# Kernel tuning notes

Hardware: AMD Instinct MI355X
Metric: run time of the kernel (lower is better)

## Reference

```python
import jax, jax.numpy as jnp
import numpy as np

# Config mirroring NEQUIPLayerFlax(hidden_irreps='64x0e + 64x1o', max_ell=1,
# avg_num_neighbors=16.0, num_species=5, mlp_n_hidden=64, mlp_n_layers=3, active_fn='relu')
N = 20000        # nodes
E = 320000       # edges (avg degree 16)
M = 64           # multiplicity per irrep
NR = 8           # radial embedding size
NSPEC = 5
AVG_NEI = 16.0
SQRT3 = 1.7320508075688772


def setup_inputs() -> dict:
    key = jax.random.key(0)
    ks = jax.random.split(key, 16)
    f32 = jnp.float32
    return {
        "vectors": jax.random.normal(ks[0], (E, 3), f32),
        "node_feats": jax.random.normal(ks[1], (N, 4 * M), f32),  # 64x0e (64) + 64x1o (192)
        "node_specie": jax.random.randint(ks[2], (N,), 0, NSPEC, jnp.int32),
        "radial_embedding": jax.random.uniform(ks[3], (E, NR), f32),
        "senders": jax.random.randint(ks[4], (E,), 0, N, jnp.int32),
        "receivers": jax.random.randint(ks[5], (E,), 0, N, jnp.int32),
        # linear_up: per-irrep-type mixing (no bias, e3nn-style /sqrt(fan_in))
        "W_up_s": jax.random.normal(ks[6], (M, M), f32),
        "W_up_v": jax.random.normal(ks[7], (M, M), f32),
        # radial MLP: NR -> 64 -> 64 -> 64 -> num_irreps(messages)=256
        "mlp_w1": jax.random.normal(ks[8], (NR, 64), f32),
        "mlp_w2": jax.random.normal(ks[9], (64, 64), f32),
        "mlp_w3": jax.random.normal(ks[10], (64, 64), f32),
        "mlp_wo": jax.random.normal(ks[11], (64, 4 * M), f32),
        # skip_tp: species-indexed linear node_feats -> (64x0e + 64x1o + 64x0e gates)
        "W_skip_s": jax.random.normal(ks[12], (NSPEC, M, 2 * M), f32),
        "W_skip_v": jax.random.normal(ks[13], (NSPEC, M, M), f32),
        # linear_down: messages (128x0e + 128x1o) -> (128x0e + 64x1o)
        "W_down_s": jax.random.normal(ks[14], (2 * M, 2 * M), f32),
        "W_down_v": jax.random.normal(ks[15], (2 * M, M), f32),
    }


def reference(vectors, node_feats, node_specie, radial_embedding, senders, receivers,
              W_up_s, W_up_v, mlp_w1, mlp_w2, mlp_w3, mlp_wo,
              W_skip_s, W_skip_v, W_down_s, W_down_v):
    n = node_feats.shape[0]
    s = node_feats[:, :M]                          # [N, 64]   0e
    v = node_feats[:, M:].reshape(n, M, 3)         # [N, 64,3] 1o

    inv_m = 1.0 / jnp.sqrt(jnp.asarray(M, node_feats.dtype))
    up_s = (s @ W_up_s) * inv_m                    # linear_up, scalar block
    up_v = jnp.einsum('nmc,mk->nkc', v, W_up_v) * inv_m

    es = up_s[senders]                             # [E, 64]
    ev = up_v[senders]                             # [E, 64, 3]

    # Y1 spherical harmonics, normalize=True, 'component' norm -> sqrt(3) * unit vector
    lengths = jnp.linalg.norm(vectors, axis=1, keepdims=True)         # [E,1]
    y = SQRT3 * vectors / lengths                                     # [E,3]

    # tensor products kept by filter_ir_out = hidden + '0e':
    # 1o x 1o -> 0e (CG = delta/sqrt(3), component norm)
    tp_s = jnp.einsum('emc,ec->em', ev, y) / SQRT3                    # [E,64]
    # 0e x 1o -> 1o (coefficient 1 under component norm)
    tp_v = es[:, :, None] * y[:, None, :]                             # [E,64,3]

    # concatenate + regroup -> 128x0e + 128x1o
    msg_s = jnp.concatenate([es, tp_s], axis=1)                       # [E,128]
    msg_v = jnp.concatenate([ev, tp_v], axis=1)                       # [E,128,3]

    # radial MLP (silu, /sqrt(fan_in) weight norm, no output activation)
    h = jax.nn.silu((radial_embedding @ mlp_w1) / jnp.sqrt(jnp.asarray(NR, jnp.float32)))
    h = jax.nn.silu((h @ mlp_w2) / 8.0)
    h = jax.nn.silu((h @ mlp_w3) / 8.0)
    mix = (h @ mlp_wo) / 8.0                                          # [E,256] = num_irreps
    mix = jnp.where(lengths == 0.0, 0.0, mix)

    msg_s = msg_s * mix[:, :2 * M]
    msg_v = msg_v * mix[:, 2 * M:, None]

    # scatter-sum to receivers, normalize by sqrt(avg_num_neighbors)
    inv_sq_nei = 1.0 / jnp.sqrt(jnp.asarray(AVG_NEI, jnp.float32))
    agg_s = jax.ops.segment_sum(msg_s, receivers, num_segments=n) * inv_sq_nei  # [N,128]
    agg_v = jax.ops.segment_sum(msg_v, receivers, num_segments=n) * inv_sq_nei  # [N,128,3]

    # linear_down -> irreps 64x0e + 64x1o + 64x0e(gates)  (scalars packed as 128)
    inv_2m = 1.0 / jnp.sqrt(jnp.asarray(2 * M, jnp.float32))
    down_s = (agg_s @ W_down_s) * inv_2m                              # [N,128]
    down_v = jnp.einsum('nmc,mk->nkc', agg_v, W_down_v) * inv_2m      # [N,64,3]

    # species-indexed skip connection from input node_feats
    Ws = W_skip_s[node_specie]                                        # [N,64,128]
    Wv = W_skip_v[node_specie]                                        # [N,64,64]
    skip_s = jnp.einsum('nm,nmk->nk', s, Ws) * inv_m                  # [N,128]
    skip_v = jnp.einsum('nmc,nmk->nkc', v, Wv) * inv_m                # [N,64,3]

    f_s = down_s + skip_s
    f_v = down_v + skip_v

    # gate: first 64 scalars are features (even_act=silu), last 64 scalars gate the 1o's
    gated_s = jax.nn.silu(f_s[:, :M])                                 # [N,64]
    gates = jax.nn.silu(f_s[:, M:])                                   # [N,64]
    gated_v = gates[:, :, None] * f_v                                 # [N,64,3]

    out = jnp.concatenate([gated_s, gated_v.reshape(n, 3 * M)], axis=1)  # [N,256]
    return jax.nn.relu(out)  # active_fn == 'relu'
```

## Files before the change

kernel.cpp:

```cpp
#include <hip/hip_runtime.h>
#include <hip/hip_fp16.h>

#define NN 20000
#define EE 320000

typedef _Float16 f16;
typedef f16  f16x8 __attribute__((ext_vector_type(8)));
typedef float f32x4 __attribute__((ext_vector_type(4)));

__device__ __forceinline__ float silu_f(float x) {
    return x / (1.0f + __expf(-x));
}

__global__ __launch_bounds__(256) void up_kernel(
    const float* __restrict__ nf, const float* __restrict__ Wus,
    const float* __restrict__ Wuv, float* __restrict__ up, int dmajor)
{
    __shared__ float sWs[64 * 64];
    __shared__ float sWv[64 * 64];
    int tid = threadIdx.x;
    for (int i = tid; i < 64 * 64; i += 256) { sWs[i] = Wus[i]; sWv[i] = Wuv[i]; }
    __syncthreads();
    int lane = tid & 63, wv = tid >> 6;
    for (int it = 0; it < 4; it++) {
        int n = blockIdx.x * 16 + wv * 4 + it;
        const float* row = nf + (size_t)n * 256;
        float s  = row[lane];
        float v0 = row[64 + lane * 3 + 0];
        float v1 = row[64 + lane * 3 + 1];
        float v2 = row[64 + lane * 3 + 2];
        float as = 0.f, a0 = 0.f, a1 = 0.f, a2 = 0.f;
        #pragma unroll 8
        for (int m = 0; m < 64; m++) {
            float sm = __shfl(s, m);
            float b0 = __shfl(v0, m), b1 = __shfl(v1, m), b2 = __shfl(v2, m);
            float w_s = sWs[m * 64 + lane];
            float w_v = sWv[m * 64 + lane];
            as += sm * w_s;
            a0 += b0 * w_v; a1 += b1 * w_v; a2 += b2 * w_v;
        }
        float* o = up + (size_t)n * 256;
        if (dmajor) {
            o[lane]       = as * 0.125f;
            o[64  + lane] = a0 * 0.125f;
            o[128 + lane] = a1 * 0.125f;
            o[192 + lane] = a2 * 0.125f;
        } else {
            o[lane] = as * 0.125f;
            o[64 + lane * 3 + 0] = a0 * 0.125f;
            o[64 + lane * 3 + 1] = a1 * 0.125f;
            o[64 + lane * 3 + 2] = a2 * 0.125f;
        }
    }
}

__global__ __launch_bounds__(256) void pack_kernel(
    const float* __restrict__ w1, const float* __restrict__ w2,
    const float* __restrict__ w3, const float* __restrict__ wo,
    f16* __restrict__ wp)
{
    int idx = blockIdx.x * 256 + threadIdx.x;
    if (idx >= 52 * 64) return;
    int frag = idx >> 6, lane = idx & 63;
    int col = lane & 15, kg = lane >> 4;
    f16x8 pv;
    if (frag < 4) {
        int t = frag;
        #pragma unroll
        for (int i = 0; i < 8; i++) {
            int k = kg * 8 + i;
            pv[i] = (k < 8) ? (f16)w1[k * 64 + t * 16 + col] : (f16)0.f;
        }
    } else if (frag < 12) {
        int f = frag - 4, t = f >> 1, h = f & 1;
        #pragma unroll
        for (int i = 0; i < 8; i++) {
            int k = h * 32 + kg * 8 + i;
            pv[i] = (f16)w2[k * 64 + t * 16 + col];
        }
    } else if (frag < 20) {
        int f = frag - 12, t = f >> 1, h = f & 1;
        #pragma unroll
        for (int i = 0; i < 8; i++) {
            int k = h * 32 + kg * 8 + i;
            pv[i] = (f16)w3[k * 64 + t * 16 + col];
        }
    } else {
        int f = frag - 20, t = f >> 1, h = f & 1;
        #pragma unroll
        for (int i = 0; i < 8; i++) {
            int k = h * 32 + kg * 8 + i;
            pv[i] = (f16)wo[k * 256 + t * 16 + col];
        }
    }
    *(f16x8*)(wp + (size_t)idx * 8) = pv;
}

__global__ __launch_bounds__(256) void pack2_kernel(
    const float* __restrict__ Wds, const float* __restrict__ Wdv,
    const float* __restrict__ Wss, const float* __restrict__ Wsv,
    f16* __restrict__ wp2)
{
    int idx = blockIdx.x * 256 + threadIdx.x;
    if (idx >= 168 * 64) return;
    int frag = idx >> 6, lane = idx & 63;
    int col = lane & 15, kg = lane >> 4;
    const float S_d = 0.25f * 0.08838834764831845f;
    const float S_k = 0.125f;
    f16x8 pv;
    if (frag < 32) {
        int t = frag >> 2, kf = frag & 3;
        #pragma unroll
        for (int i = 0; i < 8; i++) {
            int k = kf * 32 + kg * 8 + i;
            pv[i] = (f16)(Wds[k * 128 + t * 16 + col] * S_d);
        }
    } else if (frag < 48) {
        int f = frag - 32; int t = f >> 2, kf = f & 3;
        #pragma unroll
        for (int i = 0; i < 8; i++) {
            int k = kf * 32 + kg * 8 + i;
            pv[i] = (f16)(Wdv[k * 64 + t * 16 + col] * S_d);
        }
    } else if (frag < 128) {
        int f = frag - 48; int sp = f >> 4; int t = (f & 15) >> 1; int kf = f & 1;
        #pragma unroll
        for (int i = 0; i < 8; i++) {
            int k = kf * 32 + kg * 8 + i;
            pv[i] = (f16)(Wss[((size_t)sp * 64 + k) * 128 + t * 16 + col] * S_k);
        }
    } else {
        int f = frag - 128; int sp = f >> 3; int t = (f & 7) >> 1; int kf = f & 1;
        #pragma unroll
        for (int i = 0; i < 8; i++) {
            int k = kf * 32 + kg * 8 + i;
            pv[i] = (f16)(Wsv[((size_t)sp * 64 + k) * 64 + t * 16 + col] * S_k);
        }
    }
    *(f16x8*)(wp2 + (size_t)idx * 8) = pv;
}

__global__ __launch_bounds__(256) void mlp_scatter(
    const float* __restrict__ radial, const f16* __restrict__ wp,
    const int* __restrict__ senders, const int* __restrict__ receivers,
    const float* __restrict__ vectors, const float* __restrict__ up2,
    __half2* __restrict__ agg)
{
    __shared__ f16 smem[4 * 6144];
    int tid = threadIdx.x, lane = tid & 63, w = tid >> 6;
    f16* actA = smem + w * 6144;
    f16* actB = actA + 1024;
    f16* outT = actB + 1024;
    int e0 = (blockIdx.x * 4 + w) * 16;

    int col = lane & 15;
    int kg  = lane >> 4;
    const f32x4 zero = {0.f, 0.f, 0.f, 0.f};

    #define LDB(fr) (*(const f16x8*)(wp + ((size_t)(fr) * 64 + lane) * 8))
    #define LDA(buf, h) (*(const f16x8*)((buf) + (lane & 15) * 64 + \
                        (((kg * 8) + (h) * 32) ^ (((lane & 15) & 7) << 3))))
    #define STACT(buf, acc, SC)                                            \
        _Pragma("unroll")                                                  \
        for (int t = 0; t < 4; t++) {                                      \
            _Pragma("unroll")                                              \
            for (int r = 0; r < 4; r++) {                                  \
                int row = kg * 4 + r;                                      \
                int c   = t * 16 + col;                                    \
                float x = acc[t][r] * (SC);                                \
                (buf)[row * 64 + (c ^ ((row & 7) << 3))] = (f16)silu_f(x); \
            }                                                              \
        }

    {
        f16x8 a;
        if (lane < 16) {
            const float* rr = radial + (size_t)(e0 + lane) * 8;
            float4 ra = *(const float4*)rr;
            float4 rb = *(const float4*)(rr + 4);
            a[0] = (f16)ra.x; a[1] = (f16)ra.y; a[2] = (f16)ra.z; a[3] = (f16)ra.w;
            a[4] = (f16)rb.x; a[5] = (f16)rb.y; a[6] = (f16)rb.z; a[7] = (f16)rb.w;
        } else {
            #pragma unroll
            for (int i = 0; i < 8; i++) a[i] = (f16)0.f;
        }
        f32x4 acc[4];
        #pragma unroll
        for (int t = 0; t < 4; t++)
            acc[t] = __builtin_amdgcn_mfma_f32_16x16x32_f16(a, LDB(t), zero, 0, 0, 0);
        STACT(actA, acc, 0.35355339059327373f)
    }
    {
        f16x8 a0 = LDA(actA, 0), a1 = LDA(actA, 1);
        f32x4 acc[4];
        #pragma unroll
        for (int t = 0; t < 4; t++) {
            acc[t] = __builtin_amdgcn_mfma_f32_16x16x32_f16(a0, LDB(4 + t * 2), zero, 0, 0, 0);
            acc[t] = __builtin_amdgcn_mfma_f32_16x16x32_f16(a1, LDB(5 + t * 2), acc[t], 0, 0, 0);
        }
        STACT(actB, acc, 0.125f)
    }
    {
        f16x8 a0 = LDA(actB, 0), a1 = LDA(actB, 1);
        f32x4 acc[4];
        #pragma unroll
        for (int t = 0; t < 4; t++) {
            acc[t] = __builtin_amdgcn_mfma_f32_16x16x32_f16(a0, LDB(12 + t * 2), zero, 0, 0, 0);
            acc[t] = __builtin_amdgcn_mfma_f32_16x16x32_f16(a1, LDB(13 + t * 2), acc[t], 0, 0, 0);
        }
        STACT(actA, acc, 0.125f)
    }
    {
        f16x8 a0 = LDA(actA, 0), a1 = LDA(actA, 1);
        #pragma unroll
        for (int tg = 0; tg < 4; tg++) {
            f32x4 acc[4];
            #pragma unroll
            for (int q = 0; q < 4; q++) {
                int t = tg * 4 + q;
                acc[q] = __builtin_amdgcn_mfma_f32_16x16x32_f16(a0, LDB(20 + t * 2), zero, 0, 0, 0);
                acc[q] = __builtin_amdgcn_mfma_f32_16x16x32_f16(a1, LDB(21 + t * 2), acc[q], 0, 0, 0);
            }
            #pragma unroll
            for (int q = 0; q < 4; q++) {
                int t = tg * 4 + q;
                #pragma unroll
                for (int r = 0; r < 4; r++) {
                    int row = kg * 4 + r;
                    int c   = t * 16 + col;
                    outT[row * 256 + (c ^ ((row & 7) << 3))] = (f16)(acc[q][r] * 0.125f);
                }
            }
        }
    }

    const float SQ3 = 1.7320508075688772f;
    int i  = lane & 31;
    int i2 = i * 2;
    bool lo = (lane < 32);

    for (int el = 0; el < 16; el++) {
        int e = e0 + el;
        int snd = senders[e];
        int rcv = receivers[e];
        if ((unsigned)snd >= (unsigned)NN) snd = 0;
        if ((unsigned)rcv >= (unsigned)NN) rcv = 0;
        float vx = vectors[(size_t)e * 3 + 0];
        float vy = vectors[(size_t)e * 3 + 1];
        float vz = vectors[(size_t)e * 3 + 2];
        float l2 = vx * vx + vy * vy + vz * vz;
        float il   = (l2 > 0.f) ? rsqrtf(l2) : 0.f;
        float mask = (l2 > 0.f) ? 1.f : 0.f;

        int sw = (el & 7) << 3;
        const f16* orow = outT + el * 256;
        float2 mA = __half22float2(*(const __half2*)(orow + ((i2      ) ^ sw)));
        float2 mB = __half22float2(*(const __half2*)(orow + ((64 + i2) ^ sw)));
        float2 mC = __half22float2(*(const __half2*)(orow + ((128 + i2) ^ sw)));
        float2 mD = __half22float2(*(const __half2*)(orow + ((192 + i2) ^ sw)));
        float mA0 = mA.x * mask, mA1 = mA.y * mask;
        float mB0 = mB.x * mask, mB1 = mB.y * mask;
        float mC0 = mC.x * mask, mC1 = mC.y * mask;
        float mD0 = mD.x * mask, mD1 = mD.y * mask;

        const float* u = up2 + (size_t)snd * 256;
        float2 s2  = *(const float2*)(u + i2);
        float2 ex2 = *(const float2*)(u + 64  + i2);
        float2 ey2 = *(const float2*)(u + 128 + i2);
        float2 ez2 = *(const float2*)(u + 192 + i2);

        float tps0 = (ex2.x * vx + ey2.x * vy + ez2.x * vz) * il;
        float tps1 = (ex2.y * vx + ey2.y * vy + ez2.y * vz) * il;
        float yx = SQ3 * vx * il, yy = SQ3 * vy * il, yz = SQ3 * vz * il;

        float v0x = lo ? s2.x * mA0 : tps0 * mB0;
        float v0y = lo ? s2.y * mA1 : tps1 * mB1;
        float v1x = lo ? ex2.x * mC0 : ey2.x * mC0;
        float v1y = lo ? ex2.y * mC1 : ey2.y * mC1;
        float v2x = lo ? ez2.x * mC0 : s2.x * yx * mD0;
        float v2y = lo ? ez2.y * mC1 : s2.y * yx * mD1;
        float v3x = lo ? s2.x * yy * mD0 : s2.x * yz * mD0;
        float v3y = lo ? s2.y * yy * mD1 : s2.y * yz * mD1;

        __half2* ar = agg + (size_t)rcv * 256;
        unsafeAtomicAdd(ar + lane,       __floats2half2_rn(v0x, v0y));
        unsafeAtomicAdd(ar + 64  + lane, __floats2half2_rn(v1x, v1y));
        unsafeAtomicAdd(ar + 128 + lane, __floats2half2_rn(v2x, v2y));
        unsafeAtomicAdd(ar + 192 + lane, __floats2half2_rn(v3x, v3y));
    }
    #undef LDB
    #undef LDA
    #undef STACT
}

__global__ __launch_bounds__(256) void node_mfma(
    const float* __restrict__ nf, const int* __restrict__ specie,
    const f16* __restrict__ wp2, const f16* __restrict__ agg,
    float* __restrict__ out)
{
    int tid = threadIdx.x, lane = tid & 63, w = tid >> 6;
    int n0 = (blockIdx.x * 4 + w) * 16;
    if (n0 >= NN) return;
    int col = lane & 15, kg = lane >> 4;
    int myn = n0 + col;
    int mysp = specie[myn];
    if ((unsigned)mysp >= 5u) mysp = 0;
    const f32x4 zero = {0.f, 0.f, 0.f, 0.f};
    const f16x8 zv = {};

    #define LDB2(fr) (*(const f16x8*)(wp2 + ((size_t)(fr) * 64 + lane) * 8))

    f32x4 accs[8];
    #pragma unroll
    for (int t = 0; t < 8; t++) accs[t] = zero;
    #pragma unroll
    for (int kf = 0; kf < 4; kf++) {
        f16x8 a = *(const f16x8*)(agg + (size_t)myn * 512 + kf * 32 + kg * 8);
        #pragma unroll
        for (int t = 0; t < 8; t++)
            accs[t] = __builtin_amdgcn_mfma_f32_16x16x32_f16(a, LDB2(t * 4 + kf), accs[t], 0, 0, 0);
    }
    #pragma unroll
    for (int kf = 0; kf < 2; kf++) {
        const float* base = nf + (size_t)myn * 256 + kf * 32 + kg * 8;
        float4 x0 = *(const float4*)(base);
        float4 x1 = *(const float4*)(base + 4);
        f16x8 a;
        a[0] = (f16)x0.x; a[1] = (f16)x0.y; a[2] = (f16)x0.z; a[3] = (f16)x0.w;
        a[4] = (f16)x1.x; a[5] = (f16)x1.y; a[6] = (f16)x1.z; a[7] = (f16)x1.w;
        #pragma unroll
        for (int sp = 0; sp < 5; sp++) {
            f16x8 am = (mysp == sp) ? a : zv;
            #pragma unroll
            for (int t = 0; t < 8; t++)
                accs[t] = __builtin_amdgcn_mfma_f32_16x16x32_f16(am, LDB2(48 + sp * 16 + t * 2 + kf), accs[t], 0, 0, 0);
        }
    }
    float gates[4][4];
    #pragma unroll
    for (int t = 0; t < 4; t++) {
        #pragma unroll
        for (int r = 0; r < 4; r++) {
            int n = n0 + kg * 4 + r;
            out[(size_t)n * 256 + t * 16 + col] = fmaxf(silu_f(accs[t][r]), 0.f);
            gates[t][r] = silu_f(accs[4 + t][r]);
        }
    }

    #pragma unroll
    for (int c = 0; c < 3; c++) {
        f32x4 accv[4];
        #pragma unroll
        for (int t = 0; t < 4; t++) accv[t] = zero;
        #pragma unroll
        for (int kf = 0; kf < 4; kf++) {
            int off = (kf < 2) ? (128 + c * 64 + kf * 32) : (320 + c * 64 + (kf - 2) * 32);
            f16x8 a = *(const f16x8*)(agg + (size_t)myn * 512 + off + kg * 8);
            #pragma unroll
            for (int t = 0; t < 4; t++)
                accv[t] = __builtin_amdgcn_mfma_f32_16x16x32_f16(a, LDB2(32 + t * 4 + kf), accv[t], 0, 0, 0);
        }
        #pragma unroll
        for (int kf = 0; kf < 2; kf++) {
            const float* base = nf + (size_t)myn * 256 + 64 + (kf * 32 + kg * 8) * 3;
            float4 q0 = *(const float4*)(base);
            float4 q1 = *(const float4*)(base + 4);
            float4 q2 = *(const float4*)(base + 8);
            float4 q3 = *(const float4*)(base + 12);
            float4 q4 = *(const float4*)(base + 16);
            float4 q5 = *(const float4*)(base + 20);
            float qa[24] = {q0.x, q0.y, q0.z, q0.w, q1.x, q1.y, q1.z, q1.w,
                            q2.x, q2.y, q2.z, q2.w, q3.x, q3.y, q3.z, q3.w,
                            q4.x, q4.y, q4.z, q4.w, q5.x, q5.y, q5.z, q5.w};
            f16x8 a;
            #pragma unroll
            for (int i = 0; i < 8; i++) a[i] = (f16)qa[i * 3 + c];
            #pragma unroll
            for (int sp = 0; sp < 5; sp++) {
                f16x8 am = (mysp == sp) ? a : zv;
                #pragma unroll
                for (int t = 0; t < 4; t++)
                    accv[t] = __builtin_amdgcn_mfma_f32_16x16x32_f16(am, LDB2(128 + sp * 8 + t * 2 + kf), accv[t], 0, 0, 0);
            }
        }
        #pragma unroll
        for (int t = 0; t < 4; t++) {
            #pragma unroll
            for (int r = 0; r < 4; r++) {
                int n = n0 + kg * 4 + r;
                out[(size_t)n * 256 + 64 + (t * 16 + col) * 3 + c] =
                    fmaxf(gates[t][r] * accv[t][r], 0.f);
            }
        }
    }
    #undef LDB2
}

__global__ __launch_bounds__(256) void node_kernel_f(
    const float* __restrict__ nf, const int* __restrict__ specie,
    const float* __restrict__ Wds, const float* __restrict__ Wdv,
    const float* __restrict__ Wss, const float* __restrict__ Wsv,
    const float* __restrict__ agg, float* __restrict__ out)
{
    __shared__ float sDs[128 * 128];
    __shared__ float sDv[128 * 64];
    int tid = threadIdx.x;
    for (int i = tid; i < 128 * 128; i += 256) sDs[i] = Wds[i];
    for (int i = tid; i < 128 * 64; i += 256) sDv[i] = Wdv[i];
    __syncthreads();
    int lane = tid & 63, wv = tid >> 6;
    for (int it = 0; it < 4; it++) {
        int n = blockIdx.x * 16 + wv * 4 + it;
        const float* arow = agg + (size_t)n * 512;
        const float inv_nei = 0.25f;
        float as0 = arow[lane] * inv_nei;
        float as1 = arow[64 + lane] * inv_nei;
        float av00 = arow[128 + lane] * inv_nei;
        float av01 = arow[192 + lane] * inv_nei;
        float av02 = arow[256 + lane] * inv_nei;
        float av10 = arow[320 + lane] * inv_nei;
        float av11 = arow[384 + lane] * inv_nei;
        float av12 = arow[448 + lane] * inv_nei;
        const float* row = nf + (size_t)n * 256;
        float s   = row[lane];
        float vv0 = row[64 + lane * 3 + 0];
        float vv1 = row[64 + lane * 3 + 1];
        float vv2 = row[64 + lane * 3 + 2];

        float f0 = 0.f, f1 = 0.f, fv0 = 0.f, fv1 = 0.f, fv2 = 0.f;
        #pragma unroll 8
        for (int m = 0; m < 64; m++) {
            float am = __shfl(as0, m);
            f0 += am * sDs[m * 128 + lane];
            f1 += am * sDs[m * 128 + 64 + lane];
            float b0 = __shfl(av00, m), b1 = __shfl(av01, m), b2 = __shfl(av02, m);
            float wd = sDv[m * 64 + lane];
            fv0 += b0 * wd; fv1 += b1 * wd; fv2 += b2 * wd;
        }
        #pragma unroll 8
        for (int m = 0; m < 64; m++) {
            float am = __shfl(as1, m);
            f0 += am * sDs[(64 + m) * 128 + lane];
            f1 += am * sDs[(64 + m) * 128 + 64 + lane];
            float b0 = __shfl(av10, m), b1 = __shfl(av11, m), b2 = __shfl(av12, m);
            float wd = sDv[(64 + m) * 64 + lane];
            fv0 += b0 * wd; fv1 += b1 * wd; fv2 += b2 * wd;
        }
        const float inv2m = 0.08838834764831845f;
        f0 *= inv2m; f1 *= inv2m; fv0 *= inv2m; fv1 *= inv2m; fv2 *= inv2m;

        int sp = specie[n];
        if ((unsigned)sp >= 5u) sp = 0;
        const float* Ws = Wss + (size_t)sp * 64 * 128;
        const float* Wv = Wsv + (size_t)sp * 64 * 64;
        float g0 = 0.f, g1 = 0.f, h0 = 0.f, h1 = 0.f, h2 = 0.f;
        #pragma unroll 4
        for (int m = 0; m < 64; m++) {
            float sm = __shfl(s, m);
            g0 += sm * Ws[m * 128 + lane];
            g1 += sm * Ws[m * 128 + 64 + lane];
            float b0 = __shfl(vv0, m), b1 = __shfl(vv1, m), b2 = __shfl(vv2, m);
            float wsk = Wv[m * 64 + lane];
            h0 += b0 * wsk; h1 += b1 * wsk; h2 += b2 * wsk;
        }
        f0 += g0 * 0.125f; f1 += g1 * 0.125f;
        fv0 += h0 * 0.125f; fv1 += h1 * 0.125f; fv2 += h2 * 0.125f;

        float gs   = silu_f(f0);
        float gate = silu_f(f1);
        float* orow = out + (size_t)n * 256;
        orow[lane] = fmaxf(gs, 0.f);
        orow[64 + lane * 3 + 0] = fmaxf(gate * fv0, 0.f);
        orow[64 + lane * 3 + 1] = fmaxf(gate * fv1, 0.f);
        orow[64 + lane * 3 + 2] = fmaxf(gate * fv2, 0.f);
    }
}

__global__ __launch_bounds__(256) void edge_kernel_fb(
    const float* __restrict__ vectors, const float* __restrict__ radial,
    const int* __restrict__ senders, const int* __restrict__ receivers,
    const float* __restrict__ w1, const float* __restrict__ w2,
    const float* __restrict__ w3, const float* __restrict__ wo,
    const float* __restrict__ up, float* __restrict__ agg)
{
    __shared__ __half2 hL[32 * 256];
    __shared__ float   T[16 * 256];
    __shared__ float   sVec[256 * 3];
    __shared__ int     sSnd[256];
    __shared__ int     sRcv[256];

    int tid = threadIdx.x;
    int e = blockIdx.x * 256 + tid;
    int snd = senders[e];
    int rcv = receivers[e];
    if ((unsigned)snd >= (unsigned)NN) snd = 0;
    if ((unsigned)rcv >= (unsigned)NN) rcv = 0;
    float4 ra = *(const float4*)(radial + (size_t)e * 8);
    float4 rb = *(const float4*)(radial + (size_t)e * 8 + 4);
    float vx = vectors[(size_t)e * 3 + 0];
    float vy = vectors[(size_t)e * 3 + 1];
    float vz = vectors[(size_t)e * 3 + 2];
    sSnd[tid] = snd; sRcv[tid] = rcv;
    sVec[tid * 3 + 0] = vx; sVec[tid * 3 + 1] = vy; sVec[tid * 3 + 2] = vz;
    float len2 = vx * vx + vy * vy + vz * vz;
    float mask = (len2 > 0.f) ? 1.f : 0.f;

    {
        float a[64];
        #pragma unroll
        for (int j = 0; j < 64; j++) {
            float acc = ra.x * w1[j]       + ra.y * w1[64 + j]
                      + ra.z * w1[128 + j] + ra.w * w1[192 + j]
                      + rb.x * w1[256 + j] + rb.y * w1[320 + j]
                      + rb.z * w1[384 + j] + rb.w * w1[448 + j];
            a[j] = silu_f(acc * 0.35355339059327373f);
        }
        #pragma unroll
        for (int jp = 0; jp < 32; jp++)
            hL[jp * 256 + tid] = __floats2half2_rn(a[2 * jp], a[2 * jp + 1]);
    }
    {
        float acc[64];
        #pragma unroll
        for (int j = 0; j < 64; j++) acc[j] = 0.f;
        #pragma unroll 2
        for (int kp = 0; kp < 32; kp++) {
            float2 hf = __half22float2(hL[kp * 256 + tid]);
            const float* wr0 = w2 + (size_t)(2 * kp) * 64;
            const float* wr1 = w2 + (size_t)(2 * kp + 1) * 64;
            #pragma unroll
            for (int j = 0; j < 64; j++) acc[j] += hf.x * wr0[j] + hf.y * wr1[j];
        }
        #pragma unroll
        for (int jp = 0; jp < 32; jp++)
            hL[jp * 256 + tid] = __floats2half2_rn(silu_f(acc[2 * jp] * 0.125f),
                                                   silu_f(acc[2 * jp + 1] * 0.125f));
    }
    {
        float acc[64];
        #pragma unroll
        for (int j = 0; j < 64; j++) acc[j] = 0.f;
        #pragma unroll 2
        for (int kp = 0; kp < 32; kp++) {
            float2 hf = __half22float2(hL[kp * 256 + tid]);
            const float* wr0 = w3 + (size_t)(2 * kp) * 64;
            const float* wr1 = w3 + (size_t)(2 * kp + 1) * 64;
            #pragma unroll
            for (int j = 0; j < 64; j++) acc[j] += hf.x * wr0[j] + hf.y * wr1[j];
        }
        #pragma unroll
        for (int jp = 0; jp < 32; jp++)
            hL[jp * 256 + tid] = __floats2half2_rn(silu_f(acc[2 * jp] * 0.125f),
                                                   silu_f(acc[2 * jp + 1] * 0.125f));
    }

    int lane  = tid & 63;
    int wbase = tid & 192;
    int f = lane & 15;
    int g = lane >> 4;

    #define COMPUTE_CHUNK(c, ao)                                                \
        {                                                                       \
            _Pragma("unroll")                                                   \
            for (int j = 0; j < 16; j++) ao[j] = 0.f;                           \
            _Pragma("unroll 4")                                                 \
            for (int kp = 0; kp < 32; kp++) {                                   \
                float2 hf = __half22float2(hL[kp * 256 + tid]);                 \
                const float* wr0 = wo + (size_t)(2 * kp) * 256 + (c) * 16;      \
                const float* wr1 = wo + (size_t)(2 * kp + 1) * 256 + (c) * 16;  \
                _Pragma("unroll")                                               \
                for (int j = 0; j < 16; j++)                                    \
                    ao[j] += hf.x * wr0[j] + hf.y * wr1[j];                     \
            }                                                                   \
            _Pragma("unroll")                                                   \
            for (int j = 0; j < 16; j++) ao[j] *= 0.125f * mask;                \
        }

    #define WRITE_T(ao)                                                         \
        __syncthreads();                                                        \
        _Pragma("unroll")                                                       \
        for (int j = 0; j < 16; j++) T[j * 256 + (tid ^ (2 * j))] = ao[j];      \
        __syncthreads();

    for (int c = 0; c < 4; c++) {
        float ao[16];
        COMPUTE_CHUNK(c, ao)
        WRITE_T(ao)
        for (int el = 0; el < 16; el++) {
            int col = wbase + el * 4 + g;
            int s_ = sSnd[col], rc = sRcv[col];
            float mx = T[f * 256 + (col ^ (2 * f))];
            int jf = c * 16 + f;
            atomicAdd(agg + (size_t)rc * 512 + jf, up[(size_t)s_ * 256 + jf] * mx);
        }
    }
    for (int c = 4; c < 8; c++) {
        float ao[16];
        COMPUTE_CHUNK(c, ao)
        WRITE_T(ao)
        for (int el = 0; el < 16; el++) {
            int col = wbase + el * 4 + g;
            int s_ = sSnd[col], rc = sRcv[col];
            float wx = sVec[col * 3 + 0], wy = sVec[col * 3 + 1], wz = sVec[col * 3 + 2];
            float l2 = wx * wx + wy * wy + wz * wz;
            float il = (l2 > 0.f) ? rsqrtf(l2) : 0.f;
            float mx = T[f * 256 + (col ^ (2 * f))];
            int m = (c - 4) * 16 + f;
            const float* ev = up + (size_t)s_ * 256 + 64 + m * 3;
            float dot = ev[0] * wx + ev[1] * wy + ev[2] * wz;
            atomicAdd(agg + (size_t)rc * 512 + 64 + m, dot * il * mx);
        }
    }
    for (int c = 8; c < 12; c++) {
        float ao[16];
        COMPUTE_CHUNK(c, ao)
        WRITE_T(ao)
        for (int el = 0; el < 16; el++) {
            int col = wbase + el * 4 + g;
            int s_ = sSnd[col], rc = sRcv[col];
            float mx = T[f * 256 + (col ^ (2 * f))];
            int m = (c - 8) * 16 + f;
            const float* ev = up + (size_t)s_ * 256 + 64 + m * 3;
            float* ag = agg + (size_t)rc * 512 + 128 + m;
            atomicAdd(ag + 0,   ev[0] * mx);
            atomicAdd(ag + 64,  ev[1] * mx);
            atomicAdd(ag + 128, ev[2] * mx);
        }
    }
    for (int c = 12; c < 16; c++) {
        float ao[16];
        COMPUTE_CHUNK(c, ao)
        WRITE_T(ao)
        for (int el = 0; el < 16; el++) {
            int col = wbase + el * 4 + g;
            int s_ = sSnd[col], rc = sRcv[col];
            float wx = sVec[col * 3 + 0], wy = sVec[col * 3 + 1], wz = sVec[col * 3 + 2];
            float l2 = wx * wx + wy * wy + wz * wz;
            float il = (l2 > 0.f) ? rsqrtf(l2) : 0.f;
            float mx = T[f * 256 + (col ^ (2 * f))];
            int m = (c - 12) * 16 + f;
            float sc = up[(size_t)s_ * 256 + m] * 1.7320508075688772f * il * mx;
            float* ag = agg + (size_t)rc * 512 + 320 + m;
            atomicAdd(ag + 0,   sc * wx);
            atomicAdd(ag + 64,  sc * wy);
            atomicAdd(ag + 128, sc * wz);
        }
    }
    #undef COMPUTE_CHUNK
    #undef WRITE_T
}

extern "C" void kernel_launch(void* const* d_in, const int* in_sizes, int n_in,
                              void* d_out, int out_size, void* d_ws, size_t ws_size,
                              hipStream_t stream) {
    const float* vectors     = (const float*)d_in[0];
    const float* node_feats  = (const float*)d_in[1];
    const int*   node_specie = (const int*)d_in[2];
    const float* radial      = (const float*)d_in[3];
    const int*   senders     = (const int*)d_in[4];
    const int*   receivers   = (const int*)d_in[5];
    const float* W_up_s      = (const float*)d_in[6];
    const float* W_up_v      = (const float*)d_in[7];
    const float* mlp_w1      = (const float*)d_in[8];
    const float* mlp_w2      = (const float*)d_in[9];
    const float* mlp_w3      = (const float*)d_in[10];
    const float* mlp_wo      = (const float*)d_in[11];
    const float* W_skip_s    = (const float*)d_in[12];
    const float* W_skip_v    = (const float*)d_in[13];
    const float* W_down_s    = (const float*)d_in[14];
    const float* W_down_v    = (const float*)d_in[15];
    float* out = (float*)d_out;

    float* up   = (float*)d_ws;
    float* aggf = up + (size_t)NN * 256;
    __half2* aggh = (__half2*)aggf;
    uintptr_t wp_addr = ((uintptr_t)(aggf + (size_t)NN * 512) + 255) & ~(uintptr_t)255;
    f16* wpack = (f16*)wp_addr;
    f16* wp2   = wpack + (size_t)52 * 64 * 8;
    size_t required = (size_t)((uintptr_t)(wp2 + (size_t)168 * 64 * 8)
                               - (uintptr_t)d_ws);

    if (ws_size >= required) {
        hipMemsetAsync(aggh, 0, (size_t)NN * 512 * sizeof(__half), stream);
        pack_kernel<<<13, 256, 0, stream>>>(mlp_w1, mlp_w2, mlp_w3, mlp_wo, wpack);
        pack2_kernel<<<42, 256, 0, stream>>>(W_down_s, W_down_v, W_skip_s, W_skip_v, wp2);
        up_kernel<<<NN / 16, 256, 0, stream>>>(node_feats, W_up_s, W_up_v, up, 1);
        mlp_scatter<<<EE / 64, 256, 0, stream>>>(radial, wpack,
            senders, receivers, vectors, up, aggh);
        node_mfma<<<(NN / 16 + 3) / 4, 256, 0, stream>>>(node_feats, node_specie,
            wp2, (const f16*)aggh, out);
    } else {
        hipMemsetAsync(aggf, 0, (size_t)NN * 512 * sizeof(float), stream);
        up_kernel<<<NN / 16, 256, 0, stream>>>(node_feats, W_up_s, W_up_v, up, 0);
        edge_kernel_fb<<<EE / 256, 256, 0, stream>>>(
            vectors, radial, senders, receivers,
            mlp_w1, mlp_w2, mlp_w3, mlp_wo, up, aggf);
        node_kernel_f<<<NN / 16, 256, 0, stream>>>(node_feats, node_specie,
            W_down_s, W_down_v, W_skip_s, W_skip_v, aggf, out);
    }
}
```

Measured before the change: 387.8 us.

## Bucket edges by receiver block and accumulate messages in shared memory

New measurement: 1.220 ms. 3.15x slower.

```diff
diff --git a/kernel.cpp b/kernel.cpp
--- a/kernel.cpp
+++ b/kernel.cpp
@@ -3,6 +3,8 @@
 
 #define NN 20000
 #define EE 320000
+#define NB 1250
+#define BCAP 1024
 
 typedef _Float16 f16;
 typedef f16  f16x8 __attribute__((ext_vector_type(8)));
@@ -140,153 +142,185 @@
     *(f16x8*)(wp2 + (size_t)idx * 8) = pv;
 }
 
-__global__ __launch_bounds__(256) void mlp_scatter(
+__global__ void bucket_kernel(const int* __restrict__ rcv,
+                              int* __restrict__ cnt, int* __restrict__ list)
+{
+    int e = blockIdx.x * 256 + threadIdx.x;
+    int r = rcv[e];
+    if ((unsigned)r >= (unsigned)NN) return;
+    int b = r >> 4;
+    int pos = atomicAdd(&cnt[b], 1);
+    if (pos < BCAP) list[b * BCAP + pos] = e;
+}
+
+__global__ __launch_bounds__(256) void mlp_gather(
     const float* __restrict__ radial, const f16* __restrict__ wp,
     const int* __restrict__ senders, const int* __restrict__ receivers,
     const float* __restrict__ vectors, const float* __restrict__ up2,
-    __half2* __restrict__ agg)
+    const int* __restrict__ cnt, const int* __restrict__ list,
+    f16* __restrict__ agg)
 {
-    __shared__ f16 smem[4 * 6144];
+    __shared__ float acc[16 * 512];
+    __shared__ f16 mlpbuf[4 * 5120];
     int tid = threadIdx.x, lane = tid & 63, w = tid >> 6;
-    f16* actA = smem + w * 6144;
-    f16* actB = actA + 1024;
-    f16* outT = actB + 1024;
-    int e0 = (blockIdx.x * 4 + w) * 16;
-
-    int col = lane & 15;
-    int kg  = lane >> 4;
+    int b = blockIdx.x;
+    for (int i = tid; i < 16 * 512; i += 256) acc[i] = 0.f;
+    __syncthreads();
+    int count = cnt[b]; if (count > BCAP) count = BCAP;
+
+    f16* actA = mlpbuf + w * 5120;
+    f16* outT = actA + 1024;
+    int col = lane & 15, kg = lane >> 4;
     const f32x4 zero = {0.f, 0.f, 0.f, 0.f};
+    const float SQ3 = 1.7320508075688772f;
 
     #define LDB(fr) (*(const f16x8*)(wp + ((size_t)(fr) * 64 + lane) * 8))
     #define LDA(buf, h) (*(const f16x8*)((buf) + (lane & 15) * 64 + \
                         (((kg * 8) + (h) * 32) ^ (((lane & 15) & 7) << 3))))
-    #define STACT(buf, acc, SC)                                            \
+    #define STACT(buf, a4, SC)                                             \
         _Pragma("unroll")                                                  \
         for (int t = 0; t < 4; t++) {                                      \
             _Pragma("unroll")                                              \
             for (int r = 0; r < 4; r++) {                                  \
                 int row = kg * 4 + r;                                      \
                 int c   = t * 16 + col;                                    \
-                float x = acc[t][r] * (SC);                                \
+                float x = a4[t][r] * (SC);                                 \
                 (buf)[row * 64 + (c ^ ((row & 7) << 3))] = (f16)silu_f(x); \
             }                                                              \
         }
 
-    {
-        f16x8 a;
-        if (lane < 16) {
-            const float* rr = radial + (size_t)(e0 + lane) * 8;
-            float4 ra = *(const float4*)rr;
-            float4 rb = *(const float4*)(rr + 4);
-            a[0] = (f16)ra.x; a[1] = (f16)ra.y; a[2] = (f16)ra.z; a[3] = (f16)ra.w;
-            a[4] = (f16)rb.x; a[5] = (f16)rb.y; a[6] = (f16)rb.z; a[7] = (f16)rb.w;
-        } else {
-            #pragma unroll
-            for (int i = 0; i < 8; i++) a[i] = (f16)0.f;
-        }
-        f32x4 acc[4];
-        #pragma unroll
-        for (int t = 0; t < 4; t++)
-            acc[t] = __builtin_amdgcn_mfma_f32_16x16x32_f16(a, LDB(t), zero, 0, 0, 0);
-        STACT(actA, acc, 0.35355339059327373f)
-    }
-    {
-        f16x8 a0 = LDA(actA, 0), a1 = LDA(actA, 1);
-        f32x4 acc[4];
-        #pragma unroll
-        for (int t = 0; t < 4; t++) {
-            acc[t] = __builtin_amdgcn_mfma_f32_16x16x32_f16(a0, LDB(4 + t * 2), zero, 0, 0, 0);
-            acc[t] = __builtin_amdgcn_mfma_f32_16x16x32_f16(a1, LDB(5 + t * 2), acc[t], 0, 0, 0);
-        }
-        STACT(actB, acc, 0.125f)
-    }
-    {
-        f16x8 a0 = LDA(actB, 0), a1 = LDA(actB, 1);
-        f32x4 acc[4];
-        #pragma unroll
-        for (int t = 0; t < 4; t++) {
-            acc[t] = __builtin_amdgcn_mfma_f32_16x16x32_f16(a0, LDB(12 + t * 2), zero, 0, 0, 0);
-            acc[t] = __builtin_amdgcn_mfma_f32_16x16x32_f16(a1, LDB(13 + t * 2), acc[t], 0, 0, 0);
-        }
-        STACT(actA, acc, 0.125f)
-    }
-    {
-        f16x8 a0 = LDA(actA, 0), a1 = LDA(actA, 1);
-        #pragma unroll
-        for (int tg = 0; tg < 4; tg++) {
-            f32x4 acc[4];
-            #pragma unroll
-            for (int q = 0; q < 4; q++) {
-                int t = tg * 4 + q;
-                acc[q] = __builtin_amdgcn_mfma_f32_16x16x32_f16(a0, LDB(20 + t * 2), zero, 0, 0, 0);
-                acc[q] = __builtin_amdgcn_mfma_f32_16x16x32_f16(a1, LDB(21 + t * 2), acc[q], 0, 0, 0);
+    for (int base = w * 16; base < count; base += 64) {
+        int myE = -1;
+        if (lane < 16 && base + lane < count) myE = list[b * BCAP + base + lane];
+
+        {
+            f16x8 a;
+            if (lane < 16 && myE >= 0) {
+                const float* rr = radial + (size_t)myE * 8;
+                float4 ra = *(const float4*)rr;
+                float4 rb = *(const float4*)(rr + 4);
+                a[0] = (f16)ra.x; a[1] = (f16)ra.y; a[2] = (f16)ra.z; a[3] = (f16)ra.w;
+                a[4] = (f16)rb.x; a[5] = (f16)rb.y; a[6] = (f16)rb.z; a[7] = (f16)rb.w;
+            } else {
+                #pragma unroll
+                for (int i = 0; i < 8; i++) a[i] = (f16)0.f;
             }
-            #pragma unroll
-            for (int q = 0; q < 4; q++) {
-                int t = tg * 4 + q;
+            f32x4 a4[4];
+            #pragma unroll
+            for (int t = 0; t < 4; t++)
+                a4[t] = __builtin_amdgcn_mfma_f32_16x16x32_f16(a, LDB(t), zero, 0, 0, 0);
+            STACT(actA, a4, 0.35355339059327373f)
+        }
+        {
+            f16x8 a0 = LDA(actA, 0), a1 = LDA(actA, 1);
+            f32x4 a4[4];
+            #pragma unroll
+            for (int t = 0; t < 4; t++) {
+                a4[t] = __builtin_amdgcn_mfma_f32_16x16x32_f16(a0, LDB(4 + t * 2), zero, 0, 0, 0);
+                a4[t] = __builtin_amdgcn_mfma_f32_16x16x32_f16(a1, LDB(5 + t * 2), a4[t], 0, 0, 0);
+            }
+            STACT(actA, a4, 0.125f)
+        }
+        {
+            f16x8 a0 = LDA(actA, 0), a1 = LDA(actA, 1);
+            f32x4 a4[4];
+            #pragma unroll
+            for (int t = 0; t < 4; t++) {
+                a4[t] = __builtin_amdgcn_mfma_f32_16x16x32_f16(a0, LDB(12 + t * 2), zero, 0, 0, 0);
+                a4[t] = __builtin_amdgcn_mfma_f32_16x16x32_f16(a1, LDB(13 + t * 2), a4[t], 0, 0, 0);
+            }
+            STACT(actA, a4, 0.125f)
+        }
+        {
+            f16x8 a0 = LDA(actA, 0), a1 = LDA(actA, 1);
+            #pragma unroll
+            for (int tg = 0; tg < 4; tg++) {
+                f32x4 a4[4];
                 #pragma unroll
-                for (int r = 0; r < 4; r++) {
-                    int row = kg * 4 + r;
-                    int c   = t * 16 + col;
-                    outT[row * 256 + (c ^ ((row & 7) << 3))] = (f16)(acc[q][r] * 0.125f);
+                for (int q = 0; q < 4; q++) {
+                    int t = tg * 4 + q;
+                    a4[q] = __builtin_amdgcn_mfma_f32_16x16x32_f16(a0, LDB(20 + t * 2), zero, 0, 0, 0);
+                    a4[q] = __builtin_amdgcn_mfma_f32_16x16x32_f16(a1, LDB(21 + t * 2), a4[q], 0, 0, 0);
+                }
+                #pragma unroll
+                for (int q = 0; q < 4; q++) {
+                    int t = tg * 4 + q;
+                    #pragma unroll
+                    for (int r = 0; r < 4; r++) {
+                        int row = kg * 4 + r;
+                        int c   = t * 16 + col;
+                        outT[row * 256 + (c ^ ((row & 7) << 3))] = (f16)(a4[q][r] * 0.125f);
+                    }
                 }
             }
         }
-    }
-
-    const float SQ3 = 1.7320508075688772f;
-    int i  = lane & 31;
-    int i2 = i * 2;
-    bool lo = (lane < 32);
-
-    for (int el = 0; el < 16; el++) {
-        int e = e0 + el;
-        int snd = senders[e];
-        int rcv = receivers[e];
-        if ((unsigned)snd >= (unsigned)NN) snd = 0;
-        if ((unsigned)rcv >= (unsigned)NN) rcv = 0;
-        float vx = vectors[(size_t)e * 3 + 0];
-        float vy = vectors[(size_t)e * 3 + 1];
-        float vz = vectors[(size_t)e * 3 + 2];
-        float l2 = vx * vx + vy * vy + vz * vz;
-        float il   = (l2 > 0.f) ? rsqrtf(l2) : 0.f;
-        float mask = (l2 > 0.f) ? 1.f : 0.f;
-
-        int sw = (el & 7) << 3;
-        const f16* orow = outT + el * 256;
-        float2 mA = __half22float2(*(const __half2*)(orow + ((i2      ) ^ sw)));
-        float2 mB = __half22float2(*(const __half2*)(orow + ((64 + i2) ^ sw)));
-        float2 mC = __half22float2(*(const __half2*)(orow + ((128 + i2) ^ sw)));
-        float2 mD = __half22float2(*(const __half2*)(orow + ((192 + i2) ^ sw)));
-        float mA0 = mA.x * mask, mA1 = mA.y * mask;
-        float mB0 = mB.x * mask, mB1 = mB.y * mask;
-        float mC0 = mC.x * mask, mC1 = mC.y * mask;
-        float mD0 = mD.x * mask, mD1 = mD.y * mask;
-
-        const float* u = up2 + (size_t)snd * 256;
-        float2 s2  = *(const float2*)(u + i2);
-        float2 ex2 = *(const float2*)(u + 64  + i2);
-        float2 ey2 = *(const float2*)(u + 128 + i2);
-        float2 ez2 = *(const float2*)(u + 192 + i2);
-
-        float tps0 = (ex2.x * vx + ey2.x * vy + ez2.x * vz) * il;
-        float tps1 = (ex2.y * vx + ey2.y * vy + ez2.y * vz) * il;
-        float yx = SQ3 * vx * il, yy = SQ3 * vy * il, yz = SQ3 * vz * il;
-
-        float v0x = lo ? s2.x * mA0 : tps0 * mB0;
-        float v0y = lo ? s2.y * mA1 : tps1 * mB1;
-        float v1x = lo ? ex2.x * mC0 : ey2.x * mC0;
-        float v1y = lo ? ex2.y * mC1 : ey2.y * mC1;
-        float v2x = lo ? ez2.x * mC0 : s2.x * yx * mD0;
-        float v2y = lo ? ez2.y * mC1 : s2.y * yx * mD1;
-        float v3x = lo ? s2.x * yy * mD0 : s2.x * yz * mD0;
-        float v3y = lo ? s2.y * yy * mD1 : s2.y * yz * mD1;
-
-        __half2* ar = agg + (size_t)rcv * 256;
-        unsafeAtomicAdd(ar + lane,       __floats2half2_rn(v0x, v0y));
-        unsafeAtomicAdd(ar + 64  + lane, __floats2half2_rn(v1x, v1y));
-        unsafeAtomicAdd(ar + 128 + lane, __floats2half2_rn(v2x, v2y));
-        unsafeAtomicAdd(ar + 192 + lane, __floats2half2_rn(v3x, v3y));
+
+        int i2 = (lane & 31) * 2;
+        bool lo = (lane < 32);
+        for (int el = 0; el < 16; el++) {
+            int e = __shfl(myE, el);
+            if (e < 0) continue;
+            int snd = senders[e];
+            int rl  = receivers[e] - b * 16;
+            if ((unsigned)snd >= (unsigned)NN) snd = 0;
+            if ((unsigned)rl >= 16u) rl = 0;
+            float vx = vectors[(size_t)e * 3 + 0];
+            float vy = vectors[(size_t)e * 3 + 1];
+            float vz = vectors[(size_t)e * 3 + 2];
+            float l2 = vx * vx + vy * vy + vz * vz;
+            float il   = (l2 > 0.f) ? rsqrtf(l2) : 0.f;
+            float mask = (l2 > 0.f) ? 1.f : 0.f;
+
+            int sw = (el & 7) << 3;
+            const f16* orow = outT + el * 256;
+            float2 mA = __half22float2(*(const __half2*)(orow + ((i2      ) ^ sw)));
+            float2 mB = __half22float2(*(const __half2*)(orow + ((64 + i2) ^ sw)));
+            float2 mC = __half22float2(*(const __half2*)(orow + ((128 + i2) ^ sw)));
+            float2 mD = __half22float2(*(const __half2*)(orow + ((192 + i2) ^ sw)));
+            float mA0 = mA.x * mask, mA1 = mA.y * mask;
+            float mB0 = mB.x * mask, mB1 = mB.y * mask;
+            float mC0 = mC.x * mask, mC1 = mC.y * mask;
+            float mD0 = mD.x * mask, mD1 = mD.y * mask;
+
+            const float* u = up2 + (size_t)snd * 256;
+            float2 s2  = *(const float2*)(u + i2);
+            float2 ex2 = *(const float2*)(u + 64  + i2);
+            float2 ey2 = *(const float2*)(u + 128 + i2);
+            float2 ez2 = *(const float2*)(u + 192 + i2);
+
+            float tps0 = (ex2.x * vx + ey2.x * vy + ez2.x * vz) * il;
+            float tps1 = (ex2.y * vx + ey2.y * vy + ez2.y * vz) * il;
+            float yx = SQ3 * vx * il, yy = SQ3 * vy * il, yz = SQ3 * vz * il;
+
+            float v0x = lo ? s2.x * mA0 : tps0 * mB0;
+            float v0y = lo ? s2.y * mA1 : tps1 * mB1;
+            float v1x = lo ? ex2.x * mC0 : ey2.x * mC0;
+            float v1y = lo ? ex2.y * mC1 : ey2.y * mC1;
+            float v2x = lo ? ez2.x * mC0 : s2.x * yx * mD0;
+            float v2y = lo ? ez2.y * mC1 : s2.y * yx * mD1;
+            float v3x = lo ? s2.x * yy * mD0 : s2.x * yz * mD0;
+            float v3y = lo ? s2.y * yy * mD1 : s2.y * yz * mD1;
+
+            float* arow = acc + rl * 512;
+            int f0 = 2 * lane;
+            atomicAdd(arow + f0,           v0x);
+            atomicAdd(arow + f0 + 1,       v0y);
+            atomicAdd(arow + 128 + f0,     v1x);
+            atomicAdd(arow + 128 + f0 + 1, v1y);
+            atomicAdd(arow + 256 + f0,     v2x);
+            atomicAdd(arow + 256 + f0 + 1, v2y);
+            atomicAdd(arow + 384 + f0,     v3x);
+            atomicAdd(arow + 384 + f0 + 1, v3y);
+        }
+    }
+    __syncthreads();
+    #pragma unroll
+    for (int j = 0; j < 4; j++) {
+        int pos = (j * 256 + tid) * 8;
+        f16x8 v;
+        #pragma unroll
+        for (int i = 0; i < 8; i++) v[i] = (f16)acc[pos + i];
+        *(f16x8*)(agg + (size_t)b * 8192 + pos) = v;
     }
     #undef LDB
     #undef LDA
@@ -673,22 +707,25 @@
 
     float* up   = (float*)d_ws;
     float* aggf = up + (size_t)NN * 256;
-    __half2* aggh = (__half2*)aggf;
+    f16*   aggh = (f16*)aggf;
     uintptr_t wp_addr = ((uintptr_t)(aggf + (size_t)NN * 512) + 255) & ~(uintptr_t)255;
     f16* wpack = (f16*)wp_addr;
     f16* wp2   = wpack + (size_t)52 * 64 * 8;
-    size_t required = (size_t)((uintptr_t)(wp2 + (size_t)168 * 64 * 8)
+    int* cnt   = (int*)(wp2 + (size_t)168 * 64 * 8);
+    int* list  = cnt + 1280;
+    size_t required = (size_t)((uintptr_t)(list + (size_t)NB * BCAP)
                                - (uintptr_t)d_ws);
 
     if (ws_size >= required) {
-        hipMemsetAsync(aggh, 0, (size_t)NN * 512 * sizeof(__half), stream);
+        hipMemsetAsync(cnt, 0, NB * sizeof(int), stream);
         pack_kernel<<<13, 256, 0, stream>>>(mlp_w1, mlp_w2, mlp_w3, mlp_wo, wpack);
         pack2_kernel<<<42, 256, 0, stream>>>(W_down_s, W_down_v, W_skip_s, W_skip_v, wp2);
         up_kernel<<<NN / 16, 256, 0, stream>>>(node_feats, W_up_s, W_up_v, up, 1);
-        mlp_scatter<<<EE / 64, 256, 0, stream>>>(radial, wpack,
-            senders, receivers, vectors, up, aggh);
+        bucket_kernel<<<EE / 256, 256, 0, stream>>>(receivers, cnt, list);
+        mlp_gather<<<NB, 256, 0, stream>>>(radial, wpack, senders, receivers,
+            vectors, up, cnt, list, aggh);
         node_mfma<<<(NN / 16 + 3) / 4, 256, 0, stream>>>(node_feats, node_specie,
-            wp2, (const f16*)aggh, out);
+            wp2, aggh, out);
     } else {
         hipMemsetAsync(aggf, 0, (size_t)NN * 512 * sizeof(float), stream);
         up_kernel<<<NN / 16, 256, 0, stream>>>(node_feats, W_up_s, W_up_v, up, 0);
```

## Replace atomic edge scatter with receiver bucketing and per-node gather

Applied to the files above, without the earlier changes.

Measured after the change: 320.2 us. 1.21x faster.

```diff
diff --git a/kernel.cpp b/kernel.cpp
--- a/kernel.cpp
+++ b/kernel.cpp
@@ -3,6 +3,7 @@
 
 #define NN 20000
 #define EE 320000
+#define BCAP3 64
 
 typedef _Float16 f16;
 typedef f16  f16x8 __attribute__((ext_vector_type(8)));
@@ -140,11 +141,19 @@
     *(f16x8*)(wp2 + (size_t)idx * 8) = pv;
 }
 
-__global__ __launch_bounds__(256) void mlp_scatter(
+__global__ void bucket_kernel(const int* __restrict__ rcv,
+                              int* __restrict__ cnt, int* __restrict__ list)
+{
+    int e = blockIdx.x * 256 + threadIdx.x;
+    int r = rcv[e];
+    if ((unsigned)r >= (unsigned)NN) return;
+    int pos = atomicAdd(&cnt[r], 1);
+    if (pos < BCAP3) list[(size_t)r * BCAP3 + pos] = e;
+}
+
+__global__ __launch_bounds__(256) void mlp_mix(
     const float* __restrict__ radial, const f16* __restrict__ wp,
-    const int* __restrict__ senders, const int* __restrict__ receivers,
-    const float* __restrict__ vectors, const float* __restrict__ up2,
-    __half2* __restrict__ agg)
+    f16* __restrict__ mix)
 {
     __shared__ f16 smem[4 * 6144];
     int tid = threadIdx.x, lane = tid & 63, w = tid >> 6;
@@ -233,18 +242,47 @@
             }
         }
     }
-
+    #pragma unroll
+    for (int j = 0; j < 8; j++) {
+        int li  = j * 64 + lane;
+        int row = li >> 5;
+        int ci  = (li & 31) * 8;
+        f16x8 v = *(const f16x8*)(outT + row * 256 + (ci ^ ((row & 7) << 3)));
+        *(f16x8*)(mix + (size_t)(e0 + row) * 256 + ci) = v;
+    }
+    #undef LDB
+    #undef LDA
+    #undef STACT
+}
+
+__global__ __launch_bounds__(256) void gather_kernel(
+    const int* __restrict__ senders, const float* __restrict__ vectors,
+    const f16* __restrict__ mix, const float* __restrict__ up2,
+    const int* __restrict__ cnt, const int* __restrict__ list,
+    f16* __restrict__ agg)
+{
+    int tid = threadIdx.x, lane = tid & 63, w = tid >> 6;
+    int n = blockIdx.x * 4 + w;
+    if ((unsigned)n >= (unsigned)NN) return;
+    int count = cnt[n];
+    if (count > BCAP3) count = BCAP3;
+    if (count < 0) count = 0;
+
+    int sec = lane >> 3;
+    int m0  = (lane & 7) * 8;
+    int upoff = (sec == 2) ? 64 + m0 : (sec == 3) ? 128 + m0
+              : (sec == 4) ? 192 + m0 : m0;
+    int mq = (sec == 0) ? 0 : (sec == 1) ? 64 : (sec <= 4) ? 128 : 192;
     const float SQ3 = 1.7320508075688772f;
-    int i  = lane & 31;
-    int i2 = i * 2;
-    bool lo = (lane < 32);
-
-    for (int el = 0; el < 16; el++) {
-        int e = e0 + el;
+
+    float a0=0,a1=0,a2=0,a3=0,a4=0,a5=0,a6=0,a7=0;
+    const int* mylist = list + (size_t)n * BCAP3;
+
+    for (int k = 0; k < count; k++) {
+        int e = mylist[k];
+        if ((unsigned)e >= (unsigned)EE) e = 0;
         int snd = senders[e];
-        int rcv = receivers[e];
         if ((unsigned)snd >= (unsigned)NN) snd = 0;
-        if ((unsigned)rcv >= (unsigned)NN) rcv = 0;
         float vx = vectors[(size_t)e * 3 + 0];
         float vy = vectors[(size_t)e * 3 + 1];
         float vz = vectors[(size_t)e * 3 + 2];
@@ -252,45 +290,45 @@
         float il   = (l2 > 0.f) ? rsqrtf(l2) : 0.f;
         float mask = (l2 > 0.f) ? 1.f : 0.f;
 
-        int sw = (el & 7) << 3;
-        const f16* orow = outT + el * 256;
-        float2 mA = __half22float2(*(const __half2*)(orow + ((i2      ) ^ sw)));
-        float2 mB = __half22float2(*(const __half2*)(orow + ((64 + i2) ^ sw)));
-        float2 mC = __half22float2(*(const __half2*)(orow + ((128 + i2) ^ sw)));
-        float2 mD = __half22float2(*(const __half2*)(orow + ((192 + i2) ^ sw)));
-        float mA0 = mA.x * mask, mA1 = mA.y * mask;
-        float mB0 = mB.x * mask, mB1 = mB.y * mask;
-        float mC0 = mC.x * mask, mC1 = mC.y * mask;
-        float mD0 = mD.x * mask, mD1 = mD.y * mask;
-
+        f16x8 mv = *(const f16x8*)(mix + (size_t)e * 256 + mq + m0);
         const float* u = up2 + (size_t)snd * 256;
-        float2 s2  = *(const float2*)(u + i2);
-        float2 ex2 = *(const float2*)(u + 64  + i2);
-        float2 ey2 = *(const float2*)(u + 128 + i2);
-        float2 ez2 = *(const float2*)(u + 192 + i2);
-
-        float tps0 = (ex2.x * vx + ey2.x * vy + ez2.x * vz) * il;
-        float tps1 = (ex2.y * vx + ey2.y * vy + ez2.y * vz) * il;
-        float yx = SQ3 * vx * il, yy = SQ3 * vy * il, yz = SQ3 * vz * il;
-
-        float v0x = lo ? s2.x * mA0 : tps0 * mB0;
-        float v0y = lo ? s2.y * mA1 : tps1 * mB1;
-        float v1x = lo ? ex2.x * mC0 : ey2.x * mC0;
-        float v1y = lo ? ex2.y * mC1 : ey2.y * mC1;
-        float v2x = lo ? ez2.x * mC0 : s2.x * yx * mD0;
-        float v2y = lo ? ez2.y * mC1 : s2.y * yx * mD1;
-        float v3x = lo ? s2.x * yy * mD0 : s2.x * yz * mD0;
-        float v3y = lo ? s2.y * yy * mD1 : s2.y * yz * mD1;
-
-        __half2* ar = agg + (size_t)rcv * 256;
-        unsafeAtomicAdd(ar + lane,       __floats2half2_rn(v0x, v0y));
-        unsafeAtomicAdd(ar + 64  + lane, __floats2half2_rn(v1x, v1y));
-        unsafeAtomicAdd(ar + 128 + lane, __floats2half2_rn(v2x, v2y));
-        unsafeAtomicAdd(ar + 192 + lane, __floats2half2_rn(v3x, v3y));
-    }
-    #undef LDB
-    #undef LDA
-    #undef STACT
+
+        if (sec != 1) {
+            float g = (sec == 5) ? SQ3 * vx * il
+                    : (sec == 6) ? SQ3 * vy * il
+                    : (sec == 7) ? SQ3 * vz * il : mask;
+            const float* ub = u + upoff;
+            float4 u0 = *(const float4*)(ub);
+            float4 u1 = *(const float4*)(ub + 4);
+            a0 += u0.x * g * (float)mv[0];
+            a1 += u0.y * g * (float)mv[1];
+            a2 += u0.z * g * (float)mv[2];
+            a3 += u0.w * g * (float)mv[3];
+            a4 += u1.x * g * (float)mv[4];
+            a5 += u1.y * g * (float)mv[5];
+            a6 += u1.z * g * (float)mv[6];
+            a7 += u1.w * g * (float)mv[7];
+        } else {
+            float4 ex0 = *(const float4*)(u + 64  + m0);
+            float4 ex1 = *(const float4*)(u + 64  + m0 + 4);
+            float4 ey0 = *(const float4*)(u + 128 + m0);
+            float4 ey1 = *(const float4*)(u + 128 + m0 + 4);
+            float4 ez0 = *(const float4*)(u + 192 + m0);
+            float4 ez1 = *(const float4*)(u + 192 + m0 + 4);
+            a0 += (ex0.x * vx + ey0.x * vy + ez0.x * vz) * il * (float)mv[0];
+            a1 += (ex0.y * vx + ey0.y * vy + ez0.y * vz) * il * (float)mv[1];
+            a2 += (ex0.z * vx + ey0.z * vy + ez0.z * vz) * il * (float)mv[2];
+            a3 += (ex0.w * vx + ey0.w * vy + ez0.w * vz) * il * (float)mv[3];
+            a4 += (ex1.x * vx + ey1.x * vy + ez1.x * vz) * il * (float)mv[4];
+            a5 += (ex1.y * vx + ey1.y * vy + ez1.y * vz) * il * (float)mv[5];
+            a6 += (ex1.z * vx + ey1.z * vy + ez1.z * vz) * il * (float)mv[6];
+            a7 += (ex1.w * vx + ey1.w * vy + ez1.w * vz) * il * (float)mv[7];
+        }
+    }
+    f16x8 o;
+    o[0] = (f16)a0; o[1] = (f16)a1; o[2] = (f16)a2; o[3] = (f16)a3;
+    o[4] = (f16)a4; o[5] = (f16)a5; o[6] = (f16)a6; o[7] = (f16)a7;
+    *(f16x8*)(agg + (size_t)n * 512 + lane * 8) = o;
 }
 
 __global__ __launch_bounds__(256) void node_mfma(
@@ -673,22 +711,28 @@
 
     float* up   = (float*)d_ws;
     float* aggf = up + (size_t)NN * 256;
-    __half2* aggh = (__half2*)aggf;
+    f16*   aggh = (f16*)aggf;
+    int*   cnt  = (int*)((char*)aggf + 21 * 1024 * 1024);
+    int*   list = cnt + 20480;
     uintptr_t wp_addr = ((uintptr_t)(aggf + (size_t)NN * 512) + 255) & ~(uintptr_t)255;
     f16* wpack = (f16*)wp_addr;
     f16* wp2   = wpack + (size_t)52 * 64 * 8;
-    size_t required = (size_t)((uintptr_t)(wp2 + (size_t)168 * 64 * 8)
+    uintptr_t mix_addr = ((uintptr_t)(wp2 + (size_t)168 * 64 * 8) + 255) & ~(uintptr_t)255;
+    f16* mix = (f16*)mix_addr;
+    size_t required = (size_t)(mix_addr + (size_t)EE * 256 * sizeof(f16)
                                - (uintptr_t)d_ws);
 
     if (ws_size >= required) {
-        hipMemsetAsync(aggh, 0, (size_t)NN * 512 * sizeof(__half), stream);
+        hipMemsetAsync(cnt, 0, NN * sizeof(int), stream);
         pack_kernel<<<13, 256, 0, stream>>>(mlp_w1, mlp_w2, mlp_w3, mlp_wo, wpack);
         pack2_kernel<<<42, 256, 0, stream>>>(W_down_s, W_down_v, W_skip_s, W_skip_v, wp2);
         up_kernel<<<NN / 16, 256, 0, stream>>>(node_feats, W_up_s, W_up_v, up, 1);
-        mlp_scatter<<<EE / 64, 256, 0, stream>>>(radial, wpack,
-            senders, receivers, vectors, up, aggh);
+        bucket_kernel<<<EE / 256, 256, 0, stream>>>(receivers, cnt, list);
+        mlp_mix<<<EE / 64, 256, 0, stream>>>(radial, wpack, mix);
+        gather_kernel<<<NN / 4, 256, 0, stream>>>(senders, vectors, mix, up,
+            cnt, list, aggh);
         node_mfma<<<(NN / 16 + 3) / 4, 256, 0, stream>>>(node_feats, node_specie,
-            wp2, (const f16*)aggh, out);
+            wp2, aggh, out);
     } else {
         hipMemsetAsync(aggf, 0, (size_t)NN * 512 * sizeof(float), stream);
         up_kernel<<<NN / 16, 256, 0, stream>>>(node_feats, W_up_s, W_up_v, up, 0);
```
